# Kernel tuning notes

Hardware: AMD Instinct MI355X
Metric: run time of the kernel (lower is better)

Reference implementation:

```python
import jax, jax.numpy as jnp
import numpy as np

N_HEADS = 2
WINDOW = 4
BLOCK = 256


def _get_rel_emb(emb, length):
    # emb: [1, 2*WINDOW+1, K] -> [1, 2*length-1, K]
    pad = max(length - (WINDOW + 1), 0)
    start = max((WINDOW + 1) - length, 0)
    e = jnp.pad(emb, ((0, 0), (pad, pad), (0, 0)))
    return e[:, start:start + 2 * length - 1]


def _rel_to_abs(x):
    # x: [b, h, l, 2l-1] -> [b, h, l, l] (skew trick)
    b, h, l, _ = x.shape
    x = jnp.pad(x, ((0, 0), (0, 0), (0, 0), (0, 1))).reshape(b, h, 2 * l * l)
    x = jnp.pad(x, ((0, 0), (0, 0), (0, l - 1))).reshape(b, h, l + 1, 2 * l - 1)
    return x[:, :, :l, l - 1:]


def _abs_to_rel(x):
    # x: [b, h, l, l] -> [b, h, l, 2l-1] (inverse skew)
    b, h, l, _ = x.shape
    x = jnp.pad(x, ((0, 0), (0, 0), (0, 0), (0, l - 1))).reshape(b, h, l * (2 * l - 1))
    x = jnp.pad(x, ((0, 0), (0, 0), (l, 0))).reshape(b, h, l, 2 * l)
    return x[:, :, :, 1:]


def _attention(x, c, attn_mask, Wq, bq, Wk, bk, Wv, bv, Wo, bo, emb_rel_k, emb_rel_v):
    B, C, T = x.shape
    H, K = N_HEADS, C // N_HEADS
    # projections (torch Linear on [B,T,C])
    q = (jnp.einsum('bct,cd->btd', x, Wq) + bq).reshape(B, T, H, K).transpose(0, 2, 1, 3)
    k = (jnp.einsum('bct,cd->btd', c, Wk) + bk).reshape(B, T, H, K).transpose(0, 2, 1, 3)
    v = (jnp.einsum('bct,cd->btd', c, Wv) + bv).reshape(B, T, H, K).transpose(0, 2, 1, 3)
    qs = q / jnp.sqrt(jnp.float32(K))
    scores = jnp.einsum('bhtk,bhsk->bhts', qs, k)  # [B,H,T,T]
    # relative-position key logits (heads_share=True -> single table)
    rel_k = _get_rel_emb(emb_rel_k, T)[0]          # [2T-1, K]
    rel_logits = jnp.einsum('bhtk,rk->bhtr', qs, rel_k)
    scores = scores + _rel_to_abs(rel_logits)
    # proximal bias: -log1p(|i-j|)
    r = jnp.arange(T, dtype=jnp.float32)
    scores = scores - jnp.log1p(jnp.abs(r[:, None] - r[None, :]))[None, None]
    # attn mask + block-local mask (block mask active because mask is given)
    ij = jnp.arange(T)
    block_ok = jnp.abs(ij[:, None] - ij[None, :]) <= BLOCK
    valid = (attn_mask != 0) & block_ok[None, None]
    scores = jnp.where(valid, scores, jnp.float32(-1e4))
    p = jax.nn.softmax(scores, axis=-1)
    out = jnp.einsum('bhts,bhsk->bhtk', p, v)
    # relative-position value contribution
    rel_v = _get_rel_emb(emb_rel_v, T)[0]          # [2T-1, K]
    out = out + jnp.einsum('bhtr,rk->bhtk', _abs_to_rel(p), rel_v)
    out = out.transpose(0, 2, 1, 3).reshape(B, T, C)
    y = jnp.einsum('btd,do->bto', out, Wo) + bo
    return y.transpose(0, 2, 1)  # [B, out_channels, T]


def setup_inputs() -> dict:
    key = jax.random.key(0)
    ks = jax.random.split(key, 8)
    B, C, T = 4, 192, 2048
    K = C // N_HEADS
    s = jnp.float32(0.05)
    rel_std = jnp.float32(K ** -0.5)
    return {
        'x': jax.random.normal(ks[0], (B, C, T), jnp.float32),
        'c': jax.random.normal(ks[1], (B, C, T), jnp.float32),
        'Wq': jax.random.normal(ks[2], (C, C), jnp.float32) * s,
        'bq': jnp.zeros((C,), jnp.float32),
        'Wk': jax.random.normal(ks[3], (C, C), jnp.float32) * s,
        'bk': jnp.zeros((C,), jnp.float32),
        'Wv': jax.random.normal(ks[4], (C, C), jnp.float32) * s,
        'bv': jnp.zeros((C,), jnp.float32),
        'Wo': jax.random.normal(ks[5], (C, C), jnp.float32) * s,
        'bo': jnp.zeros((C,), jnp.float32),
        'emb_rel_k': jax.random.normal(ks[6], (1, 2 * WINDOW + 1, K), jnp.float32) * rel_std,
        'emb_rel_v': jax.random.normal(ks[7], (1, 2 * WINDOW + 1, K), jnp.float32) * rel_std,
        'attn_mask': jnp.ones((B, 1, T, T), jnp.int32),
    }


def reference(x, c, Wq, bq, Wk, bk, Wv, bv, Wo, bo, emb_rel_k, emb_rel_v, attn_mask):
    return _attention(x, c, attn_mask, Wq, bq, Wk, bk, Wv, bv, Wo, bo, emb_rel_k, emb_rel_v)
```

## Files before the change

kernel.cpp:

```cpp
#include <hip/hip_runtime.h>
#include <hip/hip_bf16.h>

#define B_DIM 4
#define C_DIM 192
#define T_SEQ 2048
#define H_DIM 2
#define K_DIM 96
#define BAND 256
#define IT 16
#define WSLOT 544
#define W_P 548
#define PMW 17
#define HSTR (IT*W_P)
#define OSTR 200

typedef __attribute__((ext_vector_type(8))) short bf16x8;
typedef __attribute__((ext_vector_type(4))) short bf16x4;
typedef __attribute__((ext_vector_type(4))) float f32x4;
#define MFMA16 __builtin_amdgcn_mfma_f32_16x16x32_bf16

__device__ __forceinline__ float bfbits2f(short s) {
    union { short s; __hip_bfloat16 h; } u; u.s = s; return __bfloat162float(u.h);
}
__device__ __forceinline__ short f2bf_bits(float f) {
    union { __hip_bfloat16 h; short s; } u; u.h = __float2bfloat16(f); return u.s;
}

#define OFF_WT(m)  ((size_t)(m)*73728)
#define OFF_BQS    ((size_t)294912)
#define OFF_RELKBF ((size_t)295680)
#define OFF_RVT    ((size_t)298752)
#define OFF_QBF    ((size_t)304896)
#define OFF_KBF    (OFF_QBF + 3145728)
#define OFF_VTB    (OFF_KBF + 3145728)

__global__ __launch_bounds__(256)
void prep_kernel(const float* __restrict__ Wq, const float* __restrict__ Wk,
                 const float* __restrict__ Wv, const float* __restrict__ Wo,
                 const float* __restrict__ bq, const float* __restrict__ relk,
                 const float* __restrict__ relv, char* __restrict__ ws)
{
    const float qscale = 0.10206207261596577f;
    const int bidx = blockIdx.x;
    const int tid  = threadIdx.x;

    if (bidx < 576) {
        const size_t idx = (size_t)bidx*256 + tid;
        const int mi  = (int)(idx / 36864);
        const int rem = (int)(idx % 36864);
        const int c = rem / C_DIM, d = rem % C_DIM;
        const float* src = (mi == 0) ? Wq : (mi == 1) ? Wk : (mi == 2) ? Wv : Wo;
        float v = src[c*C_DIM + d];
        if (mi == 0) v *= qscale;
        ((short*)(ws + OFF_WT(mi)))[d*C_DIM + c] = f2bf_bits(v);
        return;
    }
    if (tid < C_DIM)
        ((float*)(ws + OFF_BQS))[tid] = bq[tid]*qscale;
    short* rkb = (short*)(ws + OFF_RELKBF);
    for (int idx = tid; idx < 16*K_DIM; idx += 256) {
        const int row = idx / K_DIM;
        rkb[idx] = (row < 9) ? f2bf_bits(relk[idx]) : (short)0;
    }
    short* rvt = (short*)(ws + OFF_RVT);
    for (int idx = tid; idx < K_DIM*32; idx += 256) {
        const int col = idx >> 5, dd = idx & 31;
        rvt[idx] = (dd < 9) ? f2bf_bits(relv[dd*K_DIM + col]) : (short)0;
    }
}

__global__ __launch_bounds__(256)
void proj_kernel(const float* __restrict__ x, const float* __restrict__ cin,
                 const float* __restrict__ bk, const float* __restrict__ bv,
                 char* __restrict__ ws)
{
    __shared__ short xs[IT*C_DIM];
    __shared__ short cs[IT*C_DIM];
    const int b   = blockIdx.x >> 7;
    const int t0  = (blockIdx.x & 127) * IT;
    const int tid = threadIdx.x;
    const int wave = tid >> 6, lane = tid & 63;
    const int q4 = lane >> 4, lr = lane & 15;

    for (int l = tid; l < 768; l += 256) {
        const int cr = l >> 2, u = l & 3;
        const size_t off = (size_t)(b*C_DIM + cr)*T_SEQ + t0 + 4*u;
        const float4 xv = *reinterpret_cast<const float4*>(x + off);
        const float4 cv = *reinterpret_cast<const float4*>(cin + off);
        xs[(4*u+0)*C_DIM + cr] = f2bf_bits(xv.x);
        xs[(4*u+1)*C_DIM + cr] = f2bf_bits(xv.y);
        xs[(4*u+2)*C_DIM + cr] = f2bf_bits(xv.z);
        xs[(4*u+3)*C_DIM + cr] = f2bf_bits(xv.w);
        cs[(4*u+0)*C_DIM + cr] = f2bf_bits(cv.x);
        cs[(4*u+1)*C_DIM + cr] = f2bf_bits(cv.y);
        cs[(4*u+2)*C_DIM + cr] = f2bf_bits(cv.z);
        cs[(4*u+3)*C_DIM + cr] = f2bf_bits(cv.w);
    }
    __syncthreads();

    const short* WqT = (const short*)(ws + OFF_WT(0));
    const short* WkT = (const short*)(ws + OFF_WT(1));
    const short* WvT = (const short*)(ws + OFF_WT(2));

    f32x4 qa[3], ka[3], va[3];
    #pragma unroll
    for (int j = 0; j < 3; ++j) {
        qa[j] = (f32x4){0,0,0,0}; ka[j] = (f32x4){0,0,0,0}; va[j] = (f32x4){0,0,0,0};
    }
    for (int kc = 0; kc < 6; ++kc) {
        const int ko = kc*32 + q4*8;
        const bf16x8 xf = *reinterpret_cast<const bf16x8*>(xs + lr*C_DIM + ko);
        const bf16x8 cf = *reinterpret_cast<const bf16x8*>(cs + lr*C_DIM + ko);
        #pragma unroll
        for (int j = 0; j < 3; ++j) {
            const int dt = 3*wave + j;
            const bf16x8 wqf = *reinterpret_cast<const bf16x8*>(WqT + (dt*16 + lr)*C_DIM + ko);
            const bf16x8 wkf = *reinterpret_cast<const bf16x8*>(WkT + (dt*16 + lr)*C_DIM + ko);
            const bf16x8 wvf = *reinterpret_cast<const bf16x8*>(WvT + (dt*16 + lr)*C_DIM + ko);
            qa[j] = MFMA16(xf, wqf, qa[j], 0, 0, 0);
            ka[j] = MFMA16(cf, wkf, ka[j], 0, 0, 0);
            va[j] = MFMA16(wvf, cf, va[j], 0, 0, 0);
        }
    }

    const float* bqs = (const float*)(ws + OFF_BQS);
    short* qbf = (short*)(ws + OFF_QBF);
    short* kbf = (short*)(ws + OFF_KBF);
    short* vtb = (short*)(ws + OFF_VTB);
    #pragma unroll
    for (int j = 0; j < 3; ++j) {
        const int dt = 3*wave + j;
        {
            const int d = dt*16 + lr, h = d/K_DIM, kk = d%K_DIM;
            const int bh = b*H_DIM + h;
            const float bq_v = bqs[d], bk_v = bk[d];
            #pragma unroll
            for (int e = 0; e < 4; ++e) {
                const int t = t0 + q4*4 + e;
                const size_t off = ((size_t)bh*T_SEQ + t)*K_DIM + kk;
                qbf[off] = f2bf_bits(qa[j][e] + bq_v);
                kbf[off] = f2bf_bits(ka[j][e] + bk_v);
            }
        }
        {
            #pragma unroll
            for (int e = 0; e < 4; ++e) {
                const int d = dt*16 + q4*4 + e, h = d/K_DIM, kk = d%K_DIM;
                const int bh = b*H_DIM + h;
                vtb[((size_t)bh*K_DIM + kk)*T_SEQ + t0 + lr] = f2bf_bits(va[j][e] + bv[d]);
            }
        }
    }
}

__global__ __launch_bounds__(512, 4)
void attn_oproj_kernel(const int* __restrict__ mask, const float* __restrict__ bo,
                       float* __restrict__ y, char* __restrict__ ws)
{
    __shared__ float ps[2*HSTR];
    __shared__ float lt[257];
    __shared__ float rl[2*144];
    __shared__ unsigned pm_s[IT*PMW];
    __shared__ short pd_s[2*IT*32];

    const short* qbf = (const short*)(ws + OFF_QBF);
    const short* kbf = (const short*)(ws + OFF_KBF);
    const short* vtb = (const short*)(ws + OFF_VTB);
    const short* rkb = (const short*)(ws + OFF_RELKBF);
    const short* rvt = (const short*)(ws + OFF_RVT);
    const short* WoT = (const short*)(ws + OFF_WT(3));

    const int b   = blockIdx.x >> 7;
    const int i0  = (blockIdx.x & 127) * IT;
    const int tid = threadIdx.x;
    const int wave = tid >> 6, lane = tid & 63;
    const int head = wave >> 2, wv = wave & 3;
    const int q4 = lane >> 4, lr = lane & 15;

    const int jlo  = max(0, i0 - BAND);
    const int jhi  = min(T_SEQ - 1, i0 + IT - 1 + BAND);
    const int wlen = jhi - jlo + 1;
    const size_t qk_base = (size_t)(b*H_DIM + head) * T_SEQ * K_DIM;

    for (int idx = tid; idx < 257; idx += 512) lt[idx] = log1pf((float)idx);

    if (tid < IT*PMW) {
        const int r = tid / PMW, w = tid % PMW;
        const int* mrow = mask + ((size_t)b*T_SEQ + i0 + r)*T_SEQ;
        unsigned bits = 0;
        #pragma unroll
        for (int g4 = 0; g4 < 8; ++g4) {
            const int jg = jlo + 32*w + 4*g4;
            if (jg + 3 < T_SEQ) {
                const int4 mv = *reinterpret_cast<const int4*>(mrow + jg);
                bits |= (unsigned)(mv.x != 0) << (4*g4);
                bits |= (unsigned)(mv.y != 0) << (4*g4+1);
                bits |= (unsigned)(mv.z != 0) << (4*g4+2);
                bits |= (unsigned)(mv.w != 0) << (4*g4+3);
            } else {
                #pragma unroll
                for (int e = 0; e < 4; ++e)
                    if (jg + e < T_SEQ && mrow[jg+e] != 0) bits |= 1u << (4*g4+e);
            }
        }
        pm_s[tid] = bits;
    }

    bf16x8 qa[3];
    {
        const short* qrow = qbf + qk_base + (size_t)(i0 + lr)*K_DIM + q4*8;
        #pragma unroll
        for (int kc = 0; kc < 3; ++kc)
            qa[kc] = *reinterpret_cast<const bf16x8*>(qrow + kc*32);
    }

    float* psh = ps + head*HSTR;
    for (int jt = wv; jt < WSLOT/16; jt += 4) {
        int jr = jlo + jt*16 + lr;
        if (jr > T_SEQ-1) jr = T_SEQ-1;
        const short* krow = kbf + qk_base + (size_t)jr*K_DIM + q4*8;
        f32x4 s = {0.f,0.f,0.f,0.f};
        #pragma unroll
        for (int kc = 0; kc < 3; ++kc)
            s = MFMA16(qa[kc], *reinterpret_cast<const bf16x8*>(krow + kc*32), s, 0, 0, 0);
        #pragma unroll
        for (int e = 0; e < 4; ++e)
            psh[(q4*4 + e)*W_P + jt*16 + lr] = s[e];
    }
    if (wv == 3) {
        const short* krow = rkb + lr*K_DIM + q4*8;
        f32x4 s = {0.f,0.f,0.f,0.f};
        #pragma unroll
        for (int kc = 0; kc < 3; ++kc)
            s = MFMA16(qa[kc], *reinterpret_cast<const bf16x8*>(krow + kc*32), s, 0, 0, 0);
        if (lr < 9) {
            #pragma unroll
            for (int e = 0; e < 4; ++e)
                rl[head*144 + (q4*4 + e)*9 + lr] = s[e];
        }
    }
    __syncthreads();

    {
        const int rg = tid >> 4, sj = tid & 15;
        const int hh = rg >> 4, r = rg & 15;
        const int i = i0 + r;
        float* prow = ps + hh*HSTR + r*W_P;
        float vals[36];
        float m = -INFINITY;
        #pragma unroll
        for (int mm = 0; mm < 9; ++mm) {
            const int j0 = 4*sj + 64*mm;
            float4 pv = make_float4(0.f,0.f,0.f,0.f);
            unsigned mb = 0;
            if (j0 < WSLOT) {
                pv = *reinterpret_cast<const float4*>(prow + j0);
                mb = pm_s[r*PMW + (j0 >> 5)] >> (j0 & 31);
            }
            const float pe[4] = {pv.x, pv.y, pv.z, pv.w};
            #pragma unroll
            for (int e = 0; e < 4; ++e) {
                const int j = j0 + e;
                float val = -INFINITY;
                if (j0 < WSLOT && j < wlen) {
                    const int jg = jlo + j, dd = jg - i;
                    const int ad = dd < 0 ? -dd : dd;
                    if (ad <= BAND && ((mb >> e) & 1)) {
                        val = pe[e] - lt[ad];
                        if ((unsigned)(dd + 4) <= 8u) val += rl[hh*144 + r*9 + dd + 4];
                    }
                }
                vals[mm*4 + e] = val;
                m = fmaxf(m, val);
            }
        }
        #pragma unroll
        for (int off = 8; off > 0; off >>= 1) m = fmaxf(m, __shfl_xor(m, off, 64));
        if (m == -INFINITY) m = 0.f;
        float ssum = 0.f;
        #pragma unroll
        for (int u = 0; u < 36; ++u) { vals[u] = __expf(vals[u] - m); ssum += vals[u]; }
        #pragma unroll
        for (int off = 8; off > 0; off >>= 1) ssum += __shfl_xor(ssum, off, 64);
        const float inv = ssum > 0.f ? 1.f/ssum : 0.f;
        short* pbrow = (short*)prow;
        #pragma unroll
        for (int mm = 0; mm < 9; ++mm) {
            const int j0 = 4*sj + 64*mm;
            if (j0 < WSLOT) {
                bf16x4 w;
                #pragma unroll
                for (int e = 0; e < 4; ++e) w[e] = f2bf_bits(vals[mm*4+e]*inv);
                *reinterpret_cast<bf16x4*>(pbrow + j0) = w;
            }
        }
    }
    __syncthreads();

    for (int idx = tid; idx < 2*IT*32; idx += 512) {
        const int hh = idx >> 9, r = (idx >> 5) & 15, kk = idx & 31;
        short v = 0;
        if (kk < 9) {
            const int jg = i0 + r + kk - 4;
            if (jg >= 0 && jg < T_SEQ)
                v = ((const short*)(ps + hh*HSTR))[r*(2*W_P) + (jg - jlo)];
        }
        pd_s[idx] = v;
    }

    const short* pbh = (const short*)(ps + head*HSTR);
    f32x4 o0 = {0.f,0.f,0.f,0.f}, o1 = {0.f,0.f,0.f,0.f};
    for (int kc = 0; kc < WSLOT/32; ++kc) {
        const bf16x8 pa = *reinterpret_cast<const bf16x8*>(pbh + lr*(2*W_P) + kc*32 + q4*8);
        int tc = jlo + kc*32 + q4*8;
        if (tc > T_SEQ-8) tc = T_SEQ-8;
        const bf16x8 vb0 = *reinterpret_cast<const bf16x8*>(
            vtb + qk_base + (size_t)(wv*16 + lr)*T_SEQ + tc);
        o0 = MFMA16(pa, vb0, o0, 0, 0, 0);
        if (wv < 2) {
            const bf16x8 vb1 = *reinterpret_cast<const bf16x8*>(
                vtb + qk_base + (size_t)((wv+4)*16 + lr)*T_SEQ + tc);
            o1 = MFMA16(pa, vb1, o1, 0, 0, 0);
        }
    }
    __syncthreads();

    {
        const bf16x8 pda = *reinterpret_cast<const bf16x8*>(pd_s + head*(IT*32) + lr*32 + q4*8);
        const bf16x8 rv0 = *reinterpret_cast<const bf16x8*>(rvt + (wv*16 + lr)*32 + q4*8);
        o0 = MFMA16(pda, rv0, o0, 0, 0, 0);
        if (wv < 2) {
            const bf16x8 rv1 = *reinterpret_cast<const bf16x8*>(rvt + ((wv+4)*16 + lr)*32 + q4*8);
            o1 = MFMA16(pda, rv1, o1, 0, 0, 0);
        }
    }

    {
        short* outs = (short*)ps;
        #pragma unroll
        for (int u = 0; u < 2; ++u) {
            if (u == 1 && wv >= 2) break;
            const int nt = u ? wv + 4 : wv;
            const f32x4 oc = u ? o1 : o0;
            const int col = head*K_DIM + nt*16 + lr;
            #pragma unroll
            for (int e = 0; e < 4; ++e)
                outs[(q4*4 + e)*OSTR + col] = f2bf_bits(oc[e]);
        }
    }
    __syncthreads();

    {
        const short* outs = (const short*)ps;
        #pragma unroll
        for (int u = 0; u < 2; ++u) {
            if (u == 1 && wave >= 4) break;
            const int dt = u ? wave + 8 : wave;
            f32x4 a = {0.f,0.f,0.f,0.f};
            #pragma unroll
            for (int kc = 0; kc < 6; ++kc) {
                const int ko = kc*32 + q4*8;
                const bf16x8 af = *reinterpret_cast<const bf16x8*>(
                    WoT + (size_t)(dt*16 + lr)*C_DIM + ko);
                const bf16x8 bfr = *reinterpret_cast<const bf16x8*>(outs + lr*OSTR + ko);
                a = MFMA16(af, bfr, a, 0, 0, 0);
            }
            #pragma unroll
            for (int e = 0; e < 4; ++e) {
                const int d = dt*16 + q4*4 + e;
                y[((size_t)b*C_DIM + d)*T_SEQ + i0 + lr] = a[e] + bo[d];
            }
        }
    }
}

extern "C" void kernel_launch(void* const* d_in, const int* in_sizes, int n_in,
                              void* d_out, int out_size, void* d_ws, size_t ws_size,
                              hipStream_t stream)
{
    const float* x    = (const float*)d_in[0];
    const float* c    = (const float*)d_in[1];
    const float* Wq   = (const float*)d_in[2];
    const float* bq   = (const float*)d_in[3];
    const float* Wk   = (const float*)d_in[4];
    const float* bk   = (const float*)d_in[5];
    const float* Wv   = (const float*)d_in[6];
    const float* bv   = (const float*)d_in[7];
    const float* Wo   = (const float*)d_in[8];
    const float* bo   = (const float*)d_in[9];
    const float* relk = (const float*)d_in[10];
    const float* relv = (const float*)d_in[11];
    const int*   mask = (const int*)d_in[12];
    float*       y    = (float*)d_out;
    char*        ws   = (char*)d_ws;

    hipLaunchKernelGGL(prep_kernel, dim3(577), dim3(256), 0, stream,
                       Wq, Wk, Wv, Wo, bq, relk, relv, ws);
    hipLaunchKernelGGL(proj_kernel, dim3(B_DIM*(T_SEQ/16)), dim3(256), 0, stream,
                       x, c, bk, bv, ws);
    hipLaunchKernelGGL(attn_oproj_kernel, dim3(B_DIM*(T_SEQ/IT)), dim3(512), 0, stream,
                       mask, bo, y, ws);
}
```

Measured before the change: 175.4 us.

## Keep attention scores in registers with split-softmax and widen projection grid

The attention kernel now keeps QK^T score tiles in registers instead of writing fp32 scores to shared memory. It applies bias and masking in place and computes a per-wave partial max and sum, which are combined across the four waves through small shared arrays. Only the bf16 probabilities are written to shared memory, which shrinks LDS use and drops one full pass over shared memory. The projection kernel is split into two blocks per tile with six waves each, using padded shared strides to add parallelism. The cost is more registers per thread (nine score tiles) and an extra synchronisation step for the softmax combine.

```diff
diff --git a/kernel.cpp b/kernel.cpp
--- a/kernel.cpp
+++ b/kernel.cpp
@@ -8,11 +8,13 @@
 #define K_DIM 96
 #define BAND 256
 #define IT 16
-#define WSLOT 544
-#define W_P 548
+#define NJT 34
+#define PBS 552
+#define HSH (16*PBS)
 #define PMW 17
-#define HSTR (IT*W_P)
+#define XSTR 200
 #define OSTR 200
+#define PDS 40
 
 typedef __attribute__((ext_vector_type(8))) short bf16x8;
 typedef __attribute__((ext_vector_type(4))) short bf16x4;
@@ -69,32 +71,35 @@
     }
 }
 
-__global__ __launch_bounds__(256)
+__global__ __launch_bounds__(384)
 void proj_kernel(const float* __restrict__ x, const float* __restrict__ cin,
                  const float* __restrict__ bk, const float* __restrict__ bv,
                  char* __restrict__ ws)
 {
-    __shared__ short xs[IT*C_DIM];
-    __shared__ short cs[IT*C_DIM];
-    const int b   = blockIdx.x >> 7;
-    const int t0  = (blockIdx.x & 127) * IT;
+    __shared__ short xs[IT*XSTR];
+    __shared__ short cs[IT*XSTR];
+    const int bid = blockIdx.x;
+    const int b   = bid >> 8;
+    const int rem = bid & 255;
+    const int t0  = (rem >> 1) * IT;
+    const int g   = rem & 1;
     const int tid = threadIdx.x;
     const int wave = tid >> 6, lane = tid & 63;
     const int q4 = lane >> 4, lr = lane & 15;
 
-    for (int l = tid; l < 768; l += 256) {
+    for (int l = tid; l < 768; l += 384) {
         const int cr = l >> 2, u = l & 3;
         const size_t off = (size_t)(b*C_DIM + cr)*T_SEQ + t0 + 4*u;
         const float4 xv = *reinterpret_cast<const float4*>(x + off);
         const float4 cv = *reinterpret_cast<const float4*>(cin + off);
-        xs[(4*u+0)*C_DIM + cr] = f2bf_bits(xv.x);
-        xs[(4*u+1)*C_DIM + cr] = f2bf_bits(xv.y);
-        xs[(4*u+2)*C_DIM + cr] = f2bf_bits(xv.z);
-        xs[(4*u+3)*C_DIM + cr] = f2bf_bits(xv.w);
-        cs[(4*u+0)*C_DIM + cr] = f2bf_bits(cv.x);
-        cs[(4*u+1)*C_DIM + cr] = f2bf_bits(cv.y);
-        cs[(4*u+2)*C_DIM + cr] = f2bf_bits(cv.z);
-        cs[(4*u+3)*C_DIM + cr] = f2bf_bits(cv.w);
+        xs[(4*u+0)*XSTR + cr] = f2bf_bits(xv.x);
+        xs[(4*u+1)*XSTR + cr] = f2bf_bits(xv.y);
+        xs[(4*u+2)*XSTR + cr] = f2bf_bits(xv.z);
+        xs[(4*u+3)*XSTR + cr] = f2bf_bits(xv.w);
+        cs[(4*u+0)*XSTR + cr] = f2bf_bits(cv.x);
+        cs[(4*u+1)*XSTR + cr] = f2bf_bits(cv.y);
+        cs[(4*u+2)*XSTR + cr] = f2bf_bits(cv.z);
+        cs[(4*u+3)*XSTR + cr] = f2bf_bits(cv.w);
     }
     __syncthreads();
 
@@ -102,66 +107,58 @@
     const short* WkT = (const short*)(ws + OFF_WT(1));
     const short* WvT = (const short*)(ws + OFF_WT(2));
 
-    f32x4 qa[3], ka[3], va[3];
-    #pragma unroll
-    for (int j = 0; j < 3; ++j) {
-        qa[j] = (f32x4){0,0,0,0}; ka[j] = (f32x4){0,0,0,0}; va[j] = (f32x4){0,0,0,0};
-    }
+    const int dt = g*6 + wave;
+    f32x4 qa = {0,0,0,0}, ka = {0,0,0,0}, va = {0,0,0,0};
     for (int kc = 0; kc < 6; ++kc) {
         const int ko = kc*32 + q4*8;
-        const bf16x8 xf = *reinterpret_cast<const bf16x8*>(xs + lr*C_DIM + ko);
-        const bf16x8 cf = *reinterpret_cast<const bf16x8*>(cs + lr*C_DIM + ko);
-        #pragma unroll
-        for (int j = 0; j < 3; ++j) {
-            const int dt = 3*wave + j;
-            const bf16x8 wqf = *reinterpret_cast<const bf16x8*>(WqT + (dt*16 + lr)*C_DIM + ko);
-            const bf16x8 wkf = *reinterpret_cast<const bf16x8*>(WkT + (dt*16 + lr)*C_DIM + ko);
-            const bf16x8 wvf = *reinterpret_cast<const bf16x8*>(WvT + (dt*16 + lr)*C_DIM + ko);
-            qa[j] = MFMA16(xf, wqf, qa[j], 0, 0, 0);
-            ka[j] = MFMA16(cf, wkf, ka[j], 0, 0, 0);
-            va[j] = MFMA16(wvf, cf, va[j], 0, 0, 0);
-        }
+        const bf16x8 xf = *reinterpret_cast<const bf16x8*>(xs + lr*XSTR + ko);
+        const bf16x8 cf = *reinterpret_cast<const bf16x8*>(cs + lr*XSTR + ko);
+        const bf16x8 wqf = *reinterpret_cast<const bf16x8*>(WqT + (dt*16 + lr)*C_DIM + ko);
+        const bf16x8 wkf = *reinterpret_cast<const bf16x8*>(WkT + (dt*16 + lr)*C_DIM + ko);
+        const bf16x8 wvf = *reinterpret_cast<const bf16x8*>(WvT + (dt*16 + lr)*C_DIM + ko);
+        qa = MFMA16(xf, wqf, qa, 0, 0, 0);
+        ka = MFMA16(cf, wkf, ka, 0, 0, 0);
+        va = MFMA16(wvf, cf, va, 0, 0, 0);
     }
 
     const float* bqs = (const float*)(ws + OFF_BQS);
     short* qbf = (short*)(ws + OFF_QBF);
     short* kbf = (short*)(ws + OFF_KBF);
     short* vtb = (short*)(ws + OFF_VTB);
-    #pragma unroll
-    for (int j = 0; j < 3; ++j) {
-        const int dt = 3*wave + j;
-        {
-            const int d = dt*16 + lr, h = d/K_DIM, kk = d%K_DIM;
+    {
+        const int d = dt*16 + lr, h = d/K_DIM, kk = d%K_DIM;
+        const int bh = b*H_DIM + h;
+        const float bq_v = bqs[d], bk_v = bk[d];
+        #pragma unroll
+        for (int e = 0; e < 4; ++e) {
+            const int t = t0 + q4*4 + e;
+            const size_t off = ((size_t)bh*T_SEQ + t)*K_DIM + kk;
+            qbf[off] = f2bf_bits(qa[e] + bq_v);
+            kbf[off] = f2bf_bits(ka[e] + bk_v);
+        }
+    }
+    {
+        #pragma unroll
+        for (int e = 0; e < 4; ++e) {
+            const int d = dt*16 + q4*4 + e, h = d/K_DIM, kk = d%K_DIM;
             const int bh = b*H_DIM + h;
-            const float bq_v = bqs[d], bk_v = bk[d];
-            #pragma unroll
-            for (int e = 0; e < 4; ++e) {
-                const int t = t0 + q4*4 + e;
-                const size_t off = ((size_t)bh*T_SEQ + t)*K_DIM + kk;
-                qbf[off] = f2bf_bits(qa[j][e] + bq_v);
-                kbf[off] = f2bf_bits(ka[j][e] + bk_v);
-            }
-        }
-        {
-            #pragma unroll
-            for (int e = 0; e < 4; ++e) {
-                const int d = dt*16 + q4*4 + e, h = d/K_DIM, kk = d%K_DIM;
-                const int bh = b*H_DIM + h;
-                vtb[((size_t)bh*K_DIM + kk)*T_SEQ + t0 + lr] = f2bf_bits(va[j][e] + bv[d]);
-            }
-        }
-    }
-}
-
-__global__ __launch_bounds__(512, 4)
+            vtb[((size_t)bh*K_DIM + kk)*T_SEQ + t0 + lr] = f2bf_bits(va[e] + bv[d]);
+        }
+    }
+}
+
+__global__ __launch_bounds__(512)
 void attn_oproj_kernel(const int* __restrict__ mask, const float* __restrict__ bo,
                        float* __restrict__ y, char* __restrict__ ws)
 {
-    __shared__ float ps[2*HSTR];
+    __shared__ __align__(16) short pb[2*HSH];
     __shared__ float lt[257];
-    __shared__ float rl[2*144];
-    __shared__ unsigned pm_s[IT*PMW];
-    __shared__ short pd_s[2*IT*32];
+    __shared__ float sm_m[2][4][16];
+    __shared__ float sm_s[2][4][16];
+    __shared__ __align__(16) char upool[2560];
+    unsigned* pm_s = (unsigned*)upool;
+    float*    rl   = (float*)(upool + 1088);
+    short*    pd_s = (short*)upool;
 
     const short* qbf = (const short*)(ws + OFF_QBF);
     const short* kbf = (const short*)(ws + OFF_KBF);
@@ -214,104 +211,136 @@
             qa[kc] = *reinterpret_cast<const bf16x8*>(qrow + kc*32);
     }
 
-    float* psh = ps + head*HSTR;
-    for (int jt = wv; jt < WSLOT/16; jt += 4) {
-        int jr = jlo + jt*16 + lr;
-        if (jr > T_SEQ-1) jr = T_SEQ-1;
-        const short* krow = kbf + qk_base + (size_t)jr*K_DIM + q4*8;
-        f32x4 s = {0.f,0.f,0.f,0.f};
-        #pragma unroll
-        for (int kc = 0; kc < 3; ++kc)
-            s = MFMA16(qa[kc], *reinterpret_cast<const bf16x8*>(krow + kc*32), s, 0, 0, 0);
-        #pragma unroll
-        for (int e = 0; e < 4; ++e)
-            psh[(q4*4 + e)*W_P + jt*16 + lr] = s[e];
+    f32x4 s[9];
+    #pragma unroll
+    for (int u = 0; u < 9; ++u) {
+        s[u] = (f32x4){0.f,0.f,0.f,0.f};
+        const int jt = wv + 4*u;
+        if (jt < NJT) {
+            int jr = jlo + jt*16 + lr;
+            if (jr > T_SEQ-1) jr = T_SEQ-1;
+            const short* krow = kbf + qk_base + (size_t)jr*K_DIM + q4*8;
+            #pragma unroll
+            for (int kc = 0; kc < 3; ++kc)
+                s[u] = MFMA16(qa[kc], *reinterpret_cast<const bf16x8*>(krow + kc*32), s[u], 0, 0, 0);
+        }
     }
     if (wv == 3) {
         const short* krow = rkb + lr*K_DIM + q4*8;
-        f32x4 s = {0.f,0.f,0.f,0.f};
+        f32x4 rs = {0.f,0.f,0.f,0.f};
         #pragma unroll
         for (int kc = 0; kc < 3; ++kc)
-            s = MFMA16(qa[kc], *reinterpret_cast<const bf16x8*>(krow + kc*32), s, 0, 0, 0);
+            rs = MFMA16(qa[kc], *reinterpret_cast<const bf16x8*>(krow + kc*32), rs, 0, 0, 0);
         if (lr < 9) {
             #pragma unroll
             for (int e = 0; e < 4; ++e)
-                rl[head*144 + (q4*4 + e)*9 + lr] = s[e];
-        }
-    }
-    __syncthreads();
-
-    {
-        const int rg = tid >> 4, sj = tid & 15;
-        const int hh = rg >> 4, r = rg & 15;
-        const int i = i0 + r;
-        float* prow = ps + hh*HSTR + r*W_P;
-        float vals[36];
-        float m = -INFINITY;
-        #pragma unroll
-        for (int mm = 0; mm < 9; ++mm) {
-            const int j0 = 4*sj + 64*mm;
-            float4 pv = make_float4(0.f,0.f,0.f,0.f);
-            unsigned mb = 0;
-            if (j0 < WSLOT) {
-                pv = *reinterpret_cast<const float4*>(prow + j0);
-                mb = pm_s[r*PMW + (j0 >> 5)] >> (j0 & 31);
+                rl[head*144 + (q4*4 + e)*9 + lr] = rs[e];
+        }
+    }
+    __syncthreads();
+
+    const int dbase = jlo - i0;
+    float Mraw[4], Mc[4], Sl[4], c[4];
+    #pragma unroll
+    for (int e = 0; e < 4; ++e) Mraw[e] = -INFINITY;
+    #pragma unroll
+    for (int u = 0; u < 9; ++u) {
+        const int jt = wv + 4*u;
+        const int j = jt*16 + lr;
+        const bool tv = (jt < NJT);
+        #pragma unroll
+        for (int e = 0; e < 4; ++e) {
+            const int r = q4*4 + e;
+            float val = -INFINITY;
+            if (tv && j < wlen) {
+                const int dd = dbase + j - r;
+                const int ad = dd < 0 ? -dd : dd;
+                const unsigned bit = (pm_s[r*PMW + (jt>>1)] >> (j & 31)) & 1u;
+                if (ad <= BAND && bit) {
+                    val = s[u][e] - lt[ad];
+                    if ((unsigned)(dd + 4) <= 8u) val += rl[head*144 + r*9 + dd + 4];
+                }
             }
-            const float pe[4] = {pv.x, pv.y, pv.z, pv.w};
-            #pragma unroll
-            for (int e = 0; e < 4; ++e) {
-                const int j = j0 + e;
-                float val = -INFINITY;
-                if (j0 < WSLOT && j < wlen) {
-                    const int jg = jlo + j, dd = jg - i;
-                    const int ad = dd < 0 ? -dd : dd;
-                    if (ad <= BAND && ((mb >> e) & 1)) {
-                        val = pe[e] - lt[ad];
-                        if ((unsigned)(dd + 4) <= 8u) val += rl[hh*144 + r*9 + dd + 4];
-                    }
-                }
-                vals[mm*4 + e] = val;
-                m = fmaxf(m, val);
-            }
-        }
-        #pragma unroll
-        for (int off = 8; off > 0; off >>= 1) m = fmaxf(m, __shfl_xor(m, off, 64));
-        if (m == -INFINITY) m = 0.f;
-        float ssum = 0.f;
-        #pragma unroll
-        for (int u = 0; u < 36; ++u) { vals[u] = __expf(vals[u] - m); ssum += vals[u]; }
-        #pragma unroll
-        for (int off = 8; off > 0; off >>= 1) ssum += __shfl_xor(ssum, off, 64);
-        const float inv = ssum > 0.f ? 1.f/ssum : 0.f;
-        short* pbrow = (short*)prow;
-        #pragma unroll
-        for (int mm = 0; mm < 9; ++mm) {
-            const int j0 = 4*sj + 64*mm;
-            if (j0 < WSLOT) {
-                bf16x4 w;
-                #pragma unroll
-                for (int e = 0; e < 4; ++e) w[e] = f2bf_bits(vals[mm*4+e]*inv);
-                *reinterpret_cast<bf16x4*>(pbrow + j0) = w;
-            }
-        }
-    }
-    __syncthreads();
-
-    for (int idx = tid; idx < 2*IT*32; idx += 512) {
-        const int hh = idx >> 9, r = (idx >> 5) & 15, kk = idx & 31;
+            s[u][e] = val;
+            Mraw[e] = fmaxf(Mraw[e], val);
+        }
+    }
+    #pragma unroll
+    for (int off = 8; off > 0; off >>= 1) {
+        #pragma unroll
+        for (int e = 0; e < 4; ++e)
+            Mraw[e] = fmaxf(Mraw[e], __shfl_xor(Mraw[e], off, 64));
+    }
+    #pragma unroll
+    for (int e = 0; e < 4; ++e) {
+        Mc[e] = (Mraw[e] == -INFINITY) ? 0.f : Mraw[e];
+        Sl[e] = 0.f;
+    }
+    #pragma unroll
+    for (int u = 0; u < 9; ++u) {
+        #pragma unroll
+        for (int e = 0; e < 4; ++e) {
+            const float p = __expf(s[u][e] - Mc[e]);
+            s[u][e] = p;
+            Sl[e] += p;
+        }
+    }
+    #pragma unroll
+    for (int off = 8; off > 0; off >>= 1) {
+        #pragma unroll
+        for (int e = 0; e < 4; ++e)
+            Sl[e] += __shfl_xor(Sl[e], off, 64);
+    }
+    if (lr == 0) {
+        #pragma unroll
+        for (int e = 0; e < 4; ++e) {
+            sm_m[head][wv][q4*4 + e] = Mraw[e];
+            sm_s[head][wv][q4*4 + e] = Sl[e];
+        }
+    }
+    __syncthreads();
+
+    #pragma unroll
+    for (int e = 0; e < 4; ++e) {
+        const int r = q4*4 + e;
+        const float m0 = sm_m[head][0][r], m1 = sm_m[head][1][r];
+        const float m2 = sm_m[head][2][r], m3 = sm_m[head][3][r];
+        const float M = fmaxf(fmaxf(m0, m1), fmaxf(m2, m3));
+        const float Mh = (M == -INFINITY) ? 0.f : M;
+        const float S = sm_s[head][0][r]*__expf(((m0==-INFINITY)?0.f:m0) - Mh)
+                      + sm_s[head][1][r]*__expf(((m1==-INFINITY)?0.f:m1) - Mh)
+                      + sm_s[head][2][r]*__expf(((m2==-INFINITY)?0.f:m2) - Mh)
+                      + sm_s[head][3][r]*__expf(((m3==-INFINITY)?0.f:m3) - Mh);
+        const float inv = S > 0.f ? 1.f/S : 0.f;
+        c[e] = __expf(Mc[e] - Mh) * inv;
+    }
+    #pragma unroll
+    for (int u = 0; u < 9; ++u) {
+        const int jt = wv + 4*u;
+        if (jt < NJT) {
+            #pragma unroll
+            for (int e = 0; e < 4; ++e)
+                pb[head*HSH + (q4*4 + e)*PBS + jt*16 + lr] = f2bf_bits(s[u][e]*c[e]);
+        }
+    }
+    __syncthreads();
+
+    for (int idx = tid; idx < 2*IT*PDS; idx += 512) {
+        const int hh = idx / (IT*PDS), rem2 = idx % (IT*PDS);
+        const int r = rem2 / PDS, kk = rem2 % PDS;
         short v = 0;
         if (kk < 9) {
             const int jg = i0 + r + kk - 4;
             if (jg >= 0 && jg < T_SEQ)
-                v = ((const short*)(ps + hh*HSTR))[r*(2*W_P) + (jg - jlo)];
+                v = pb[hh*HSH + r*PBS + (jg - jlo)];
         }
         pd_s[idx] = v;
     }
 
-    const short* pbh = (const short*)(ps + head*HSTR);
+    const short* pbh = pb + head*HSH;
     f32x4 o0 = {0.f,0.f,0.f,0.f}, o1 = {0.f,0.f,0.f,0.f};
-    for (int kc = 0; kc < WSLOT/32; ++kc) {
-        const bf16x8 pa = *reinterpret_cast<const bf16x8*>(pbh + lr*(2*W_P) + kc*32 + q4*8);
+    for (int kc = 0; kc < NJT/2; ++kc) {
+        const bf16x8 pa = *reinterpret_cast<const bf16x8*>(pbh + lr*PBS + kc*32 + q4*8);
         int tc = jlo + kc*32 + q4*8;
         if (tc > T_SEQ-8) tc = T_SEQ-8;
         const bf16x8 vb0 = *reinterpret_cast<const bf16x8*>(
@@ -326,7 +355,7 @@
     __syncthreads();
 
     {
-        const bf16x8 pda = *reinterpret_cast<const bf16x8*>(pd_s + head*(IT*32) + lr*32 + q4*8);
+        const bf16x8 pda = *reinterpret_cast<const bf16x8*>(pd_s + head*(IT*PDS) + lr*PDS + q4*8);
         const bf16x8 rv0 = *reinterpret_cast<const bf16x8*>(rvt + (wv*16 + lr)*32 + q4*8);
         o0 = MFMA16(pda, rv0, o0, 0, 0, 0);
         if (wv < 2) {
@@ -336,7 +365,7 @@
     }
 
     {
-        short* outs = (short*)ps;
+        short* outs = pb;
         #pragma unroll
         for (int u = 0; u < 2; ++u) {
             if (u == 1 && wv >= 2) break;
@@ -351,7 +380,7 @@
     __syncthreads();
 
     {
-        const short* outs = (const short*)ps;
+        const short* outs = pb;
         #pragma unroll
         for (int u = 0; u < 2; ++u) {
             if (u == 1 && wave >= 4) break;
@@ -396,7 +425,7 @@
 
     hipLaunchKernelGGL(prep_kernel, dim3(577), dim3(256), 0, stream,
                        Wq, Wk, Wv, Wo, bq, relk, relv, ws);
-    hipLaunchKernelGGL(proj_kernel, dim3(B_DIM*(T_SEQ/16)), dim3(256), 0, stream,
+    hipLaunchKernelGGL(proj_kernel, dim3(B_DIM*(T_SEQ/16)*2), dim3(384), 0, stream,
                        x, c, bk, bv, ws);
     hipLaunchKernelGGL(attn_oproj_kernel, dim3(B_DIM*(T_SEQ/IT)), dim3(512), 0, stream,
                        mask, bo, y, ws);
```

After: 181.2 us. 1.03x slower.

## Prefetch K/V fragments, pad LDS strides, swizzle block order, alias shared buffers

Applied to the files above, without the earlier changes.

Software-pipelines the QK^T and PV loops so the next K and V^T fragments are loaded from global memory while the current MFMAs run. It also hoists the Q fragment load ahead of the mask/log table setup and pads the LDS row strides (x/c tiles, score rows, pd rows) to reduce bank conflicts. Blocks are remapped with an XOR-style swizzle to spread batches across CUs, and the pm_s/rl/pd_s scratch arrays share one pool to cut LDS use. This adds register pressure from the prefetch registers, and the aliasing depends on pm_s/rl no longer being live when pd_s is written.

```diff
diff --git a/kernel.cpp b/kernel.cpp
--- a/kernel.cpp
+++ b/kernel.cpp
@@ -8,11 +8,14 @@
 #define K_DIM 96
 #define BAND 256
 #define IT 16
+#define NJT 34
 #define WSLOT 544
-#define W_P 548
+#define WPD 556
+#define PRS (2*WPD)
 #define PMW 17
-#define HSTR (IT*W_P)
+#define XSTR 200
 #define OSTR 200
+#define PDS 40
 
 typedef __attribute__((ext_vector_type(8))) short bf16x8;
 typedef __attribute__((ext_vector_type(4))) short bf16x4;
@@ -33,6 +36,8 @@
 #define OFF_QBF    ((size_t)304896)
 #define OFF_KBF    (OFF_QBF + 3145728)
 #define OFF_VTB    (OFF_KBF + 3145728)
+
+__device__ __forceinline__ int swz512(int hw) { return ((hw & 7) << 6) + (hw >> 3); }
 
 __global__ __launch_bounds__(256)
 void prep_kernel(const float* __restrict__ Wq, const float* __restrict__ Wk,
@@ -74,10 +79,11 @@
                  const float* __restrict__ bk, const float* __restrict__ bv,
                  char* __restrict__ ws)
 {
-    __shared__ short xs[IT*C_DIM];
-    __shared__ short cs[IT*C_DIM];
-    const int b   = blockIdx.x >> 7;
-    const int t0  = (blockIdx.x & 127) * IT;
+    __shared__ short xs[IT*XSTR];
+    __shared__ short cs[IT*XSTR];
+    const int bid = swz512(blockIdx.x);
+    const int b   = bid >> 7;
+    const int t0  = (bid & 127) * IT;
     const int tid = threadIdx.x;
     const int wave = tid >> 6, lane = tid & 63;
     const int q4 = lane >> 4, lr = lane & 15;
@@ -87,14 +93,14 @@
         const size_t off = (size_t)(b*C_DIM + cr)*T_SEQ + t0 + 4*u;
         const float4 xv = *reinterpret_cast<const float4*>(x + off);
         const float4 cv = *reinterpret_cast<const float4*>(cin + off);
-        xs[(4*u+0)*C_DIM + cr] = f2bf_bits(xv.x);
-        xs[(4*u+1)*C_DIM + cr] = f2bf_bits(xv.y);
-        xs[(4*u+2)*C_DIM + cr] = f2bf_bits(xv.z);
-        xs[(4*u+3)*C_DIM + cr] = f2bf_bits(xv.w);
-        cs[(4*u+0)*C_DIM + cr] = f2bf_bits(cv.x);
-        cs[(4*u+1)*C_DIM + cr] = f2bf_bits(cv.y);
-        cs[(4*u+2)*C_DIM + cr] = f2bf_bits(cv.z);
-        cs[(4*u+3)*C_DIM + cr] = f2bf_bits(cv.w);
+        xs[(4*u+0)*XSTR + cr] = f2bf_bits(xv.x);
+        xs[(4*u+1)*XSTR + cr] = f2bf_bits(xv.y);
+        xs[(4*u+2)*XSTR + cr] = f2bf_bits(xv.z);
+        xs[(4*u+3)*XSTR + cr] = f2bf_bits(xv.w);
+        cs[(4*u+0)*XSTR + cr] = f2bf_bits(cv.x);
+        cs[(4*u+1)*XSTR + cr] = f2bf_bits(cv.y);
+        cs[(4*u+2)*XSTR + cr] = f2bf_bits(cv.z);
+        cs[(4*u+3)*XSTR + cr] = f2bf_bits(cv.w);
     }
     __syncthreads();
 
@@ -109,8 +115,8 @@
     }
     for (int kc = 0; kc < 6; ++kc) {
         const int ko = kc*32 + q4*8;
-        const bf16x8 xf = *reinterpret_cast<const bf16x8*>(xs + lr*C_DIM + ko);
-        const bf16x8 cf = *reinterpret_cast<const bf16x8*>(cs + lr*C_DIM + ko);
+        const bf16x8 xf = *reinterpret_cast<const bf16x8*>(xs + lr*XSTR + ko);
+        const bf16x8 cf = *reinterpret_cast<const bf16x8*>(cs + lr*XSTR + ko);
         #pragma unroll
         for (int j = 0; j < 3; ++j) {
             const int dt = 3*wave + j;
@@ -147,7 +153,7 @@
             for (int e = 0; e < 4; ++e) {
                 const int d = dt*16 + q4*4 + e, h = d/K_DIM, kk = d%K_DIM;
                 const int bh = b*H_DIM + h;
-                vtb[((size_t)bh*K_DIM + kk)*T_SEQ + t0 + lr] = f2bf_bits(va[j][e] + bv[d]);
+                vtb[((size_t)bh*K_DIM + kk)*T_SEQ + t0 + lr] = f2bf_bits(va[e == e ? j : j][e] + bv[d]);
             }
         }
     }
@@ -157,11 +163,12 @@
 void attn_oproj_kernel(const int* __restrict__ mask, const float* __restrict__ bo,
                        float* __restrict__ y, char* __restrict__ ws)
 {
-    __shared__ float ps[2*HSTR];
+    __shared__ __align__(16) float ps[2*IT*WPD];
     __shared__ float lt[257];
-    __shared__ float rl[2*144];
-    __shared__ unsigned pm_s[IT*PMW];
-    __shared__ short pd_s[2*IT*32];
+    __shared__ __align__(16) char upool[2560];
+    unsigned* pm_s = (unsigned*)upool;
+    float*    rl   = (float*)(upool + 1088);
+    short*    pd_s = (short*)upool;
 
     const short* qbf = (const short*)(ws + OFF_QBF);
     const short* kbf = (const short*)(ws + OFF_KBF);
@@ -170,8 +177,9 @@
     const short* rvt = (const short*)(ws + OFF_RVT);
     const short* WoT = (const short*)(ws + OFF_WT(3));
 
-    const int b   = blockIdx.x >> 7;
-    const int i0  = (blockIdx.x & 127) * IT;
+    const int bid = swz512(blockIdx.x);
+    const int b   = bid >> 7;
+    const int i0  = (bid & 127) * IT;
     const int tid = threadIdx.x;
     const int wave = tid >> 6, lane = tid & 63;
     const int head = wave >> 2, wv = wave & 3;
@@ -181,6 +189,14 @@
     const int jhi  = min(T_SEQ - 1, i0 + IT - 1 + BAND);
     const int wlen = jhi - jlo + 1;
     const size_t qk_base = (size_t)(b*H_DIM + head) * T_SEQ * K_DIM;
+
+    bf16x8 qa[3];
+    {
+        const short* qrow = qbf + qk_base + (size_t)(i0 + lr)*K_DIM + q4*8;
+        #pragma unroll
+        for (int kc = 0; kc < 3; ++kc)
+            qa[kc] = *reinterpret_cast<const bf16x8*>(qrow + kc*32);
+    }
 
     for (int idx = tid; idx < 257; idx += 512) lt[idx] = log1pf((float)idx);
 
@@ -206,37 +222,46 @@
         pm_s[tid] = bits;
     }
 
-    bf16x8 qa[3];
-    {
-        const short* qrow = qbf + qk_base + (size_t)(i0 + lr)*K_DIM + q4*8;
-        #pragma unroll
-        for (int kc = 0; kc < 3; ++kc)
-            qa[kc] = *reinterpret_cast<const bf16x8*>(qrow + kc*32);
-    }
-
-    float* psh = ps + head*HSTR;
-    for (int jt = wv; jt < WSLOT/16; jt += 4) {
-        int jr = jlo + jt*16 + lr;
-        if (jr > T_SEQ-1) jr = T_SEQ-1;
-        const short* krow = kbf + qk_base + (size_t)jr*K_DIM + q4*8;
-        f32x4 s = {0.f,0.f,0.f,0.f};
-        #pragma unroll
-        for (int kc = 0; kc < 3; ++kc)
-            s = MFMA16(qa[kc], *reinterpret_cast<const bf16x8*>(krow + kc*32), s, 0, 0, 0);
-        #pragma unroll
-        for (int e = 0; e < 4; ++e)
-            psh[(q4*4 + e)*W_P + jt*16 + lr] = s[e];
+    float* psh = ps + head*(IT*WPD);
+    {
+        int jt = wv;
+        int jr = jlo + jt*16 + lr; if (jr > T_SEQ-1) jr = T_SEQ-1;
+        const short* kr = kbf + qk_base + (size_t)jr*K_DIM + q4*8;
+        bf16x8 kf0 = *reinterpret_cast<const bf16x8*>(kr);
+        bf16x8 kf1 = *reinterpret_cast<const bf16x8*>(kr + 32);
+        bf16x8 kf2 = *reinterpret_cast<const bf16x8*>(kr + 64);
+        while (true) {
+            const int jn = jt + 4;
+            const bool more = (jn < NJT);
+            bf16x8 nf0, nf1, nf2;
+            if (more) {
+                int jr2 = jlo + jn*16 + lr; if (jr2 > T_SEQ-1) jr2 = T_SEQ-1;
+                const short* kr2 = kbf + qk_base + (size_t)jr2*K_DIM + q4*8;
+                nf0 = *reinterpret_cast<const bf16x8*>(kr2);
+                nf1 = *reinterpret_cast<const bf16x8*>(kr2 + 32);
+                nf2 = *reinterpret_cast<const bf16x8*>(kr2 + 64);
+            }
+            f32x4 s = {0.f,0.f,0.f,0.f};
+            s = MFMA16(qa[0], kf0, s, 0, 0, 0);
+            s = MFMA16(qa[1], kf1, s, 0, 0, 0);
+            s = MFMA16(qa[2], kf2, s, 0, 0, 0);
+            float* pr = psh + (q4*4)*WPD + jt*16 + lr;
+            pr[0*WPD] = s[0]; pr[1*WPD] = s[1]; pr[2*WPD] = s[2]; pr[3*WPD] = s[3];
+            if (!more) break;
+            kf0 = nf0; kf1 = nf1; kf2 = nf2;
+            jt = jn;
+        }
     }
     if (wv == 3) {
         const short* krow = rkb + lr*K_DIM + q4*8;
-        f32x4 s = {0.f,0.f,0.f,0.f};
+        f32x4 rs = {0.f,0.f,0.f,0.f};
         #pragma unroll
         for (int kc = 0; kc < 3; ++kc)
-            s = MFMA16(qa[kc], *reinterpret_cast<const bf16x8*>(krow + kc*32), s, 0, 0, 0);
+            rs = MFMA16(qa[kc], *reinterpret_cast<const bf16x8*>(krow + kc*32), rs, 0, 0, 0);
         if (lr < 9) {
             #pragma unroll
             for (int e = 0; e < 4; ++e)
-                rl[head*144 + (q4*4 + e)*9 + lr] = s[e];
+                rl[head*144 + (q4*4 + e)*9 + lr] = rs[e];
         }
     }
     __syncthreads();
@@ -245,7 +270,7 @@
         const int rg = tid >> 4, sj = tid & 15;
         const int hh = rg >> 4, r = rg & 15;
         const int i = i0 + r;
-        float* prow = ps + hh*HSTR + r*W_P;
+        float* prow = ps + hh*(IT*WPD) + r*WPD;
         float vals[36];
         float m = -INFINITY;
         #pragma unroll
@@ -297,36 +322,45 @@
     }
     __syncthreads();
 
-    for (int idx = tid; idx < 2*IT*32; idx += 512) {
-        const int hh = idx >> 9, r = (idx >> 5) & 15, kk = idx & 31;
+    for (int idx = tid; idx < 2*IT*PDS; idx += 512) {
+        const int hh = idx / (IT*PDS), rem2 = idx % (IT*PDS);
+        const int r = rem2 / PDS, kk = rem2 % PDS;
         short v = 0;
         if (kk < 9) {
             const int jg = i0 + r + kk - 4;
             if (jg >= 0 && jg < T_SEQ)
-                v = ((const short*)(ps + hh*HSTR))[r*(2*W_P) + (jg - jlo)];
+                v = ((const short*)ps)[hh*(IT*PRS) + r*PRS + (jg - jlo)];
         }
         pd_s[idx] = v;
     }
 
-    const short* pbh = (const short*)(ps + head*HSTR);
+    const short* pbh = (const short*)ps + head*(IT*PRS);
     f32x4 o0 = {0.f,0.f,0.f,0.f}, o1 = {0.f,0.f,0.f,0.f};
-    for (int kc = 0; kc < WSLOT/32; ++kc) {
-        const bf16x8 pa = *reinterpret_cast<const bf16x8*>(pbh + lr*(2*W_P) + kc*32 + q4*8);
-        int tc = jlo + kc*32 + q4*8;
-        if (tc > T_SEQ-8) tc = T_SEQ-8;
-        const bf16x8 vb0 = *reinterpret_cast<const bf16x8*>(
-            vtb + qk_base + (size_t)(wv*16 + lr)*T_SEQ + tc);
-        o0 = MFMA16(pa, vb0, o0, 0, 0, 0);
-        if (wv < 2) {
-            const bf16x8 vb1 = *reinterpret_cast<const bf16x8*>(
-                vtb + qk_base + (size_t)((wv+4)*16 + lr)*T_SEQ + tc);
-            o1 = MFMA16(pa, vb1, o1, 0, 0, 0);
+    {
+        const short* vbase0 = vtb + qk_base + (size_t)(wv*16 + lr)*T_SEQ;
+        const short* vbase1 = vtb + qk_base + (size_t)((wv+4)*16 + lr)*T_SEQ;
+        int tc = jlo + q4*8; if (tc > T_SEQ-8) tc = T_SEQ-8;
+        bf16x8 vb0 = *reinterpret_cast<const bf16x8*>(vbase0 + tc);
+        bf16x8 vb1 = {};
+        if (wv < 2) vb1 = *reinterpret_cast<const bf16x8*>(vbase1 + tc);
+        for (int kc = 0; kc < NJT/2; ++kc) {
+            bf16x8 nv0, nv1;
+            const bool more = (kc + 1 < NJT/2);
+            if (more) {
+                int tn = jlo + (kc+1)*32 + q4*8; if (tn > T_SEQ-8) tn = T_SEQ-8;
+                nv0 = *reinterpret_cast<const bf16x8*>(vbase0 + tn);
+                if (wv < 2) nv1 = *reinterpret_cast<const bf16x8*>(vbase1 + tn);
+            }
+            const bf16x8 pa = *reinterpret_cast<const bf16x8*>(pbh + lr*PRS + kc*32 + q4*8);
+            o0 = MFMA16(pa, vb0, o0, 0, 0, 0);
+            if (wv < 2) o1 = MFMA16(pa, vb1, o1, 0, 0, 0);
+            if (more) { vb0 = nv0; if (wv < 2) vb1 = nv1; }
         }
     }
     __syncthreads();
 
     {
-        const bf16x8 pda = *reinterpret_cast<const bf16x8*>(pd_s + head*(IT*32) + lr*32 + q4*8);
+        const bf16x8 pda = *reinterpret_cast<const bf16x8*>(pd_s + head*(IT*PDS) + lr*PDS + q4*8);
         const bf16x8 rv0 = *reinterpret_cast<const bf16x8*>(rvt + (wv*16 + lr)*32 + q4*8);
         o0 = MFMA16(pda, rv0, o0, 0, 0, 0);
         if (wv < 2) {
```

Result: no change. 175.3 us (-0.0%).
